# Kernel optimization log

Measured on AMD Instinct MI355X. Metric: run time of the kernel, lower is better.

Reference implementation:

```python
import jax, jax.numpy as jnp
import numpy as np

IN_F, OUT_F = 1024, 1024
GRID_SIZE, SPLINE_ORDER = 5, 3
GRID_RANGE = (-1.0, 1.0)
NUM_BASIS = GRID_SIZE + SPLINE_ORDER  # 8


def b_splines(x, grid, spline_order):
    # x: (B, in), grid: (in, G) with G = grid_size + 2*spline_order + 1
    x = x[..., None]            # (B, in, 1)
    g = grid[None, :, :]        # (1, in, G)
    B = ((x >= g[..., :-1]) & (x < g[..., 1:])).astype(x.dtype)  # (B, in, G-1)
    for k in range(1, spline_order + 1):
        left = (x - g[..., :-(k + 1)]) / (g[..., k:-1] - g[..., :-(k + 1)])
        right = (g[..., k + 1:] - x) / (g[..., k + 1:] - g[..., 1:-k])
        B = left * B[..., :-1] + right * B[..., 1:]
    return B  # (B, in, grid_size + spline_order)


def setup_inputs() -> dict:
    key = jax.random.key(0)
    k1, k2, k3, k4 = jax.random.split(key, 4)
    batch = 8192
    x = jax.random.normal(k1, (batch, IN_F), dtype=jnp.float32)
    h = (GRID_RANGE[1] - GRID_RANGE[0]) / GRID_SIZE
    knots = jnp.arange(-SPLINE_ORDER, GRID_SIZE + SPLINE_ORDER + 1, dtype=jnp.float32) * h + GRID_RANGE[0]
    grid = jnp.broadcast_to(knots, (IN_F, knots.shape[0]))  # (in, 12)
    base_weight = jax.random.normal(k2, (OUT_F, IN_F), dtype=jnp.float32) * (1.0 / np.sqrt(IN_F))
    spline_weight = jax.random.normal(k3, (OUT_F, IN_F, NUM_BASIS), dtype=jnp.float32) * 0.02
    spline_scaler = jax.random.normal(k4, (OUT_F, IN_F), dtype=jnp.float32) * (1.0 / np.sqrt(IN_F))
    return {"x": x, "grid": grid, "base_weight": base_weight,
            "spline_weight": spline_weight, "spline_scaler": spline_scaler}


def reference(x, grid, base_weight, spline_weight, spline_scaler):
    # base branch: SiLU then linear
    base_out = jax.nn.silu(x) @ base_weight.T  # (B, out)
    # normalize x to [-1, 1] by global min/max
    x_min, x_max = jnp.min(x), jnp.max(x)
    x_norm = (x - x_min) / (x_max - x_min + 1e-8) * 2.0 - 1.0
    basis = b_splines(x_norm, grid, SPLINE_ORDER)  # (B, in, K)
    w = spline_weight * spline_scaler[..., None]   # (out, in, K)
    spline_out = jnp.einsum('bik,oik->bo', basis, w)
    return base_out + spline_out
```

## Files before the change

kernel.cpp:

```cpp
#include <hip/hip_runtime.h>
#include <hip/hip_bf16.h>

#define IN_F   1024
#define OUT_F  1024
#define NBASIS 8
#define KDIM   (IN_F + IN_F * NBASIS)
#define BK 64
#define KT      (KDIM / BK)

#define BM3 128
#define BN3 256
#define A_ELEMS (BM3 * BK)
#define B_ELEMS (BN3 * BK)
#define SLOT    (A_ELEMS + B_ELEMS)
#define A_OFF   0
#define B_OFF   A_ELEMS

#define BM 128
#define BN 128

typedef __attribute__((ext_vector_type(8)))  short          bf16x8;
typedef __attribute__((ext_vector_type(8)))  unsigned short u16x8;
typedef __attribute__((ext_vector_type(4)))  float          f32x4;
typedef __attribute__((ext_vector_type(16))) float          f32x16;

typedef const __attribute__((address_space(1))) void gas_t;
typedef __attribute__((address_space(3))) void las_t;
#define GLD16(g, l) __builtin_amdgcn_global_load_lds((gas_t*)(g), (las_t*)(l), 16, 0, 0)

__device__ __forceinline__ unsigned short bfr(float f) {
    unsigned u = __float_as_uint(f);
    unsigned r = (u + 0x7FFFu + ((u >> 16) & 1u)) >> 16;
    return (unsigned short)r;
}
__device__ __forceinline__ float silu_f(float v) { return v / (1.0f + __expf(-v)); }

__device__ __forceinline__ unsigned fkey(float f) {
    unsigned u = __float_as_uint(f);
    return u ^ ((u >> 31) ? 0xFFFFFFFFu : 0x80000000u);
}
__device__ __forceinline__ float fkey_dec(unsigned u) {
    unsigned b = (u >> 31) ? (u ^ 0x80000000u) : ~u;
    return __uint_as_float(b);
}

__device__ __forceinline__ void spline8(float xv, float xmin, float scale, u16x8* o8p) {
    float xn = (xv - xmin) * scale - 1.0f;
    float u  = (xn + 2.2f) * 2.5f;
    int   iv = (int)floorf(u);
    iv = iv < 3 ? 3 : (iv > 7 ? 7 : iv);
    float tt = u - (float)iv;
    float s1 = 1.0f - tt;
    float t2 = tt * tt, t3 = t2 * tt;
    float n0 = s1 * s1 * s1 * (1.0f / 6.0f);
    float n1 = (3.0f * t3 - 6.0f * t2 + 4.0f) * (1.0f / 6.0f);
    float n2 = (-3.0f * t3 + 3.0f * t2 + 3.0f * tt + 1.0f) * (1.0f / 6.0f);
    float n3 = t3 * (1.0f / 6.0f);
    int j0 = iv - 3;
    u16x8 o8;
    #pragma unroll
    for (int s = 0; s < 8; ++s) {
        int d = s - j0;
        float val = (d == 0) ? n0 : (d == 1) ? n1 : (d == 2) ? n2 : (d == 3) ? n3 : 0.0f;
        o8[s] = bfr(val);
    }
    *o8p = o8;
}

__global__ void k_minmax(const float* __restrict__ x, unsigned* __restrict__ mm, int n4) {
    int tid    = blockIdx.x * blockDim.x + threadIdx.x;
    int stride = gridDim.x * blockDim.x;
    const float4* x4 = (const float4*)x;
    float mx  = -3.402823466e+38f;
    float mxn = -3.402823466e+38f;
    for (int i = tid; i < n4; i += stride) {
        float4 v = x4[i];
        mx  = fmaxf(mx,  fmaxf(fmaxf(v.x, v.y), fmaxf(v.z, v.w)));
        mxn = fmaxf(mxn, -fminf(fminf(v.x, v.y), fminf(v.z, v.w)));
    }
    #pragma unroll
    for (int off = 32; off; off >>= 1) {
        mx  = fmaxf(mx,  __shfl_down(mx,  off));
        mxn = fmaxf(mxn, __shfl_down(mxn, off));
    }
    __shared__ float smx[4], smn[4];
    int lane = threadIdx.x & 63, wid = threadIdx.x >> 6;
    if (lane == 0) { smx[wid] = mx; smn[wid] = mxn; }
    __syncthreads();
    if (threadIdx.x == 0) {
        #pragma unroll
        for (int w = 1; w < 4; ++w) { mx = fmaxf(mx, smx[w]); mxn = fmaxf(mxn, smn[w]); }
        atomicMax(&mm[0], fkey(mx));
        atomicMax(&mm[1], fkey(mxn));
    }
}

__global__ void k_prep_all(const float* __restrict__ x, const unsigned* __restrict__ mm,
                           const float* __restrict__ bw, const float* __restrict__ sw,
                           const float* __restrict__ sc,
                           unsigned short* __restrict__ Ac, unsigned short* __restrict__ Wc,
                           int nba) {
    int bid = blockIdx.x;
    if (bid < nba) {
        int t = bid * 256 + threadIdx.x;
        int row = t >> 10, i = t & 1023;
        const float xmax  = fkey_dec(mm[0]);
        const float xmin  = -fkey_dec(mm[1]);
        const float scale = 2.0f / (xmax - xmin + 1e-8f);
        float xv = x[t];
        size_t rb = (size_t)row * KDIM;
        Ac[rb + i] = bfr(silu_f(xv));
        u16x8 o8;
        spline8(xv, xmin, scale, &o8);
        *(u16x8*)(Ac + rb + IN_F + (size_t)i * 8) = o8;
    } else {
        int t = (bid - nba) * 256 + threadIdx.x;
        int o = t >> 10, i = t & 1023;
        Wc[(size_t)o * KDIM + i] = bfr(bw[t]);
        float s = sc[t];
        const float4* swv = (const float4*)(sw + (size_t)t * 8);
        float4 a = swv[0], b = swv[1];
        u16x8 o8;
        o8[0] = bfr(a.x * s); o8[1] = bfr(a.y * s); o8[2] = bfr(a.z * s); o8[3] = bfr(a.w * s);
        o8[4] = bfr(b.x * s); o8[5] = bfr(b.y * s); o8[6] = bfr(b.z * s); o8[7] = bfr(b.w * s);
        *(u16x8*)(Wc + (size_t)o * KDIM + IN_F + i * 8) = o8;
    }
}

#define MFMA32(a, b, c) __builtin_amdgcn_mfma_f32_32x32x16_bf16((a), (b), (c), 0, 0, 0)
#define MFMA16(a, b, c) __builtin_amdgcn_mfma_f32_16x16x32_bf16((a), (b), (c), 0, 0, 0)

__global__ __launch_bounds__(512, 2)
void k_gemm4(const unsigned short* __restrict__ Ac, const unsigned short* __restrict__ Wc,
             float* __restrict__ out) {
    __shared__ unsigned short sm[3 * SLOT];

    const int t    = threadIdx.x;
    const int lane = t & 63, w = t >> 6;
    const int bid  = blockIdx.x;
    const int xcd = bid & 7, s = bid >> 3;
    const int bM  = xcd * 8 + (s & 7);
    const int bN  = s >> 3;

    const int wave_r = w >> 2;
    const int wcq    = w & 3;
    const int l31 = lane & 31;
    const int hl  = lane >> 5;

    const unsigned short* pa0; const unsigned short* pa1;
    const unsigned short* pb0; const unsigned short* pb1;
    const unsigned short* pb2; const unsigned short* pb3;
    {
        int L, r, c;
        L = (0 * 8 + w) * 64 + lane; r = L >> 3; c = L & 7;
        pa0 = Ac + (size_t)(bM * BM3 + r) * KDIM + (c ^ (r & 7)) * 8;
        L = (1 * 8 + w) * 64 + lane; r = L >> 3; c = L & 7;
        pa1 = Ac + (size_t)(bM * BM3 + r) * KDIM + (c ^ (r & 7)) * 8;
        L = (0 * 8 + w) * 64 + lane; r = L >> 3; c = L & 7;
        pb0 = Wc + (size_t)(bN * BN3 + r) * KDIM + (c ^ (r & 7)) * 8;
        L = (1 * 8 + w) * 64 + lane; r = L >> 3; c = L & 7;
        pb1 = Wc + (size_t)(bN * BN3 + r) * KDIM + (c ^ (r & 7)) * 8;
        L = (2 * 8 + w) * 64 + lane; r = L >> 3; c = L & 7;
        pb2 = Wc + (size_t)(bN * BN3 + r) * KDIM + (c ^ (r & 7)) * 8;
        L = (3 * 8 + w) * 64 + lane; r = L >> 3; c = L & 7;
        pb3 = Wc + (size_t)(bN * BN3 + r) * KDIM + (c ^ (r & 7)) * 8;
    }

    int rA[2], rB[2];
    #pragma unroll
    for (int mi = 0; mi < 2; ++mi) rA[mi] = wave_r * 64 + mi * 32 + l31;
    #pragma unroll
    for (int ni = 0; ni < 2; ++ni) rB[ni] = wcq * 64 + ni * 32 + l31;

    f32x16 acc[2][2] = {};

    GLD16(pa0, &sm[0 * SLOT + A_OFF + (0 * 8 + w) * 512]);
    GLD16(pa1, &sm[0 * SLOT + A_OFF + (1 * 8 + w) * 512]);
    GLD16(pb0, &sm[0 * SLOT + B_OFF + (0 * 8 + w) * 512]);
    GLD16(pb1, &sm[0 * SLOT + B_OFF + (1 * 8 + w) * 512]);
    GLD16(pb2, &sm[0 * SLOT + B_OFF + (2 * 8 + w) * 512]);
    GLD16(pb3, &sm[0 * SLOT + B_OFF + (3 * 8 + w) * 512]);
    pa0 += BK; pa1 += BK; pb0 += BK; pb1 += BK; pb2 += BK; pb3 += BK;
    GLD16(pa0, &sm[1 * SLOT + A_OFF + (0 * 8 + w) * 512]);
    GLD16(pa1, &sm[1 * SLOT + A_OFF + (1 * 8 + w) * 512]);
    GLD16(pb0, &sm[1 * SLOT + B_OFF + (0 * 8 + w) * 512]);
    GLD16(pb1, &sm[1 * SLOT + B_OFF + (1 * 8 + w) * 512]);
    GLD16(pb2, &sm[1 * SLOT + B_OFF + (2 * 8 + w) * 512]);
    GLD16(pb3, &sm[1 * SLOT + B_OFF + (3 * 8 + w) * 512]);
    pa0 += BK; pa1 += BK; pb0 += BK; pb1 += BK; pb2 += BK; pb3 += BK;

    int o0 = 0, o1 = SLOT, o2 = 2 * SLOT;
    int sk = 2;

    asm volatile("s_waitcnt vmcnt(6)" ::: "memory");
    asm volatile("s_barrier" ::: "memory");

    for (int kt = 0; kt < KT; ++kt) {
        {
            bf16x8 a0[2], a1[2], b0[2], b1[2];
            #pragma unroll
            for (int mi = 0; mi < 2; ++mi) {
                int sa = rA[mi] & 7;
                a0[mi] = *(const bf16x8*)&sm[o0 + A_OFF + rA[mi] * BK + (((0 + hl) ^ sa) << 3)];
                a1[mi] = *(const bf16x8*)&sm[o0 + A_OFF + rA[mi] * BK + (((2 + hl) ^ sa) << 3)];
            }
            #pragma unroll
            for (int ni = 0; ni < 2; ++ni) {
                int sb = rB[ni] & 7;
                b0[ni] = *(const bf16x8*)&sm[o0 + B_OFF + rB[ni] * BK + (((0 + hl) ^ sb) << 3)];
                b1[ni] = *(const bf16x8*)&sm[o0 + B_OFF + rB[ni] * BK + (((2 + hl) ^ sb) << 3)];
            }
            GLD16(pa0, &sm[o2 + A_OFF + (0 * 8 + w) * 512]);
            GLD16(pa1, &sm[o2 + A_OFF + (1 * 8 + w) * 512]);
            __builtin_amdgcn_s_barrier();
            __builtin_amdgcn_s_setprio(1);
            #pragma unroll
            for (int mi = 0; mi < 2; ++mi)
                #pragma unroll
                for (int ni = 0; ni < 2; ++ni) {
                    acc[mi][ni] = MFMA32(a0[mi], b0[ni], acc[mi][ni]);
                    acc[mi][ni] = MFMA32(a1[mi], b1[ni], acc[mi][ni]);
                }
            __builtin_amdgcn_s_setprio(0);
            __builtin_amdgcn_s_barrier();
        }
        {
            bf16x8 a0[2], a1[2], b0[2], b1[2];
            #pragma unroll
            for (int mi = 0; mi < 2; ++mi) {
                int sa = rA[mi] & 7;
                a0[mi] = *(const bf16x8*)&sm[o0 + A_OFF + rA[mi] * BK + (((4 + hl) ^ sa) << 3)];
                a1[mi] = *(const bf16x8*)&sm[o0 + A_OFF + rA[mi] * BK + (((6 + hl) ^ sa) << 3)];
            }
            #pragma unroll
            for (int ni = 0; ni < 2; ++ni) {
                int sb = rB[ni] & 7;
                b0[ni] = *(const bf16x8*)&sm[o0 + B_OFF + rB[ni] * BK + (((4 + hl) ^ sb) << 3)];
                b1[ni] = *(const bf16x8*)&sm[o0 + B_OFF + rB[ni] * BK + (((6 + hl) ^ sb) << 3)];
            }
            GLD16(pb0, &sm[o2 + B_OFF + (0 * 8 + w) * 512]);
            GLD16(pb1, &sm[o2 + B_OFF + (1 * 8 + w) * 512]);
            GLD16(pb2, &sm[o2 + B_OFF + (2 * 8 + w) * 512]);
            GLD16(pb3, &sm[o2 + B_OFF + (3 * 8 + w) * 512]);
            __builtin_amdgcn_s_barrier();
            __builtin_amdgcn_s_setprio(1);
            #pragma unroll
            for (int mi = 0; mi < 2; ++mi)
                #pragma unroll
                for (int ni = 0; ni < 2; ++ni) {
                    acc[mi][ni] = MFMA32(a0[mi], b0[ni], acc[mi][ni]);
                    acc[mi][ni] = MFMA32(a1[mi], b1[ni], acc[mi][ni]);
                }
            __builtin_amdgcn_s_setprio(0);
        }

        pa0 += BK; pa1 += BK; pb0 += BK; pb1 += BK; pb2 += BK; pb3 += BK;
        if (++sk == KT) {
            sk = 0;
            pa0 -= KDIM; pa1 -= KDIM; pb0 -= KDIM; pb1 -= KDIM; pb2 -= KDIM; pb3 -= KDIM;
        }

        asm volatile("s_waitcnt vmcnt(6)" ::: "memory");
        asm volatile("s_barrier" ::: "memory");
        int tmp = o0; o0 = o1; o1 = o2; o2 = tmp;
    }

    #pragma unroll
    for (int mi = 0; mi < 2; ++mi) {
        #pragma unroll
        for (int ni = 0; ni < 2; ++ni) {
            #pragma unroll
            for (int reg = 0; reg < 16; ++reg) {
                int row = bM * BM3 + wave_r * 64 + mi * 32 + (reg & 3) + 8 * (reg >> 2) + 4 * hl;
                int col = bN * BN3 + wcq * 64 + ni * 32 + l31;
                out[(size_t)row * OUT_F + col] = acc[mi][ni][reg];
            }
        }
    }
}

__global__ __launch_bounds__(256, 2)
void k_gemm2(const unsigned short* __restrict__ Ac, const unsigned short* __restrict__ Wc,
             float* __restrict__ out, int nmb) {
    __shared__ unsigned short As[BM * BK];
    __shared__ unsigned short Bs[BN * BK];

    const int t = threadIdx.x;
    const int lane = t & 63, w = t >> 6;
    int bid = blockIdx.x;
    int bM = bid >> 3, bN = bid & 7;

    const unsigned short* pa[4];
    const unsigned short* pb[4];
    #pragma unroll
    for (int q = 0; q < 4; ++q) {
        int idx = (q * 4 + w) * 64 + lane;
        int r = idx >> 3, c8 = idx & 7;
        pa[q] = Ac + (size_t)(bM * BM + r) * KDIM + c8 * 8;
        pb[q] = Wc + (size_t)(bN * BN + r) * KDIM + c8 * 8;
    }

    const int wr  = (w >> 1) * 64;
    const int wc2 = (w & 1) * 64;

    f32x4 acc[4][4] = {};

    for (int kt = 0; kt < KT; ++kt) {
        __syncthreads();
        #pragma unroll
        for (int q = 0; q < 4; ++q) {
            GLD16(pa[q], &As[(q * 4 + w) * 512]);
            GLD16(pb[q], &Bs[(q * 4 + w) * 512]);
            pa[q] += BK;
            pb[q] += BK;
        }
        __syncthreads();

        bf16x8 af[4][2];
        #pragma unroll
        for (int mi = 0; mi < 4; ++mi) {
            int row = wr + mi * 16 + (lane & 15);
            #pragma unroll
            for (int ks = 0; ks < 2; ++ks)
                af[mi][ks] = *(const bf16x8*)&As[row * BK + ks * 32 + (lane >> 4) * 8];
        }
        #pragma unroll
        for (int ni = 0; ni < 4; ++ni) {
            int col = wc2 + ni * 16 + (lane & 15);
            bf16x8 b0 = *(const bf16x8*)&Bs[col * BK + (lane >> 4) * 8];
            bf16x8 b1 = *(const bf16x8*)&Bs[col * BK + 32 + (lane >> 4) * 8];
            #pragma unroll
            for (int mi = 0; mi < 4; ++mi) {
                acc[mi][ni] = MFMA16(af[mi][0], b0, acc[mi][ni]);
                acc[mi][ni] = MFMA16(af[mi][1], b1, acc[mi][ni]);
            }
        }
    }

    #pragma unroll
    for (int mi = 0; mi < 4; ++mi) {
        #pragma unroll
        for (int ni = 0; ni < 4; ++ni) {
            #pragma unroll
            for (int reg = 0; reg < 4; ++reg) {
                int row = wr + mi * 16 + (lane >> 4) * 4 + reg;
                int col = wc2 + ni * 16 + (lane & 15);
                out[(size_t)(bM * BM + row) * OUT_F + bN * BN + col] = acc[mi][ni][reg];
            }
        }
    }
}

extern "C" void kernel_launch(void* const* d_in, const int* in_sizes, int n_in,
                              void* d_out, int out_size, void* d_ws, size_t ws_size,
                              hipStream_t stream) {
    const float* x  = (const float*)d_in[0];
    const float* bw = (const float*)d_in[2];
    const float* sw = (const float*)d_in[3];
    const float* sc = (const float*)d_in[4];
    float* out = (float*)d_out;

    const int batch = in_sizes[0] / IN_F;
    const int n4    = in_sizes[0] / 4;

    unsigned*       mm = (unsigned*)d_ws;
    unsigned short* Wc = (unsigned short*)((char*)d_ws + 512);
    const size_t    wc_bytes = (size_t)OUT_F * KDIM * 2;
    unsigned short* Ac = (unsigned short*)((char*)d_ws + 512 + wc_bytes);
    const size_t    ac_bytes = (size_t)batch * KDIM * 2;
    const size_t    need = 512 + wc_bytes + ac_bytes;

    hipMemsetAsync(d_ws, 0, 8, stream);
    k_minmax<<<1024, 256, 0, stream>>>(x, mm, n4);

    const int nba = (batch * IN_F) / 256;
    k_prep_all<<<nba + (OUT_F * IN_F) / 256, 256, 0, stream>>>(x, mm, bw, sw, sc, Ac, Wc, nba);

    if (ws_size >= need && batch == 8192) {
        k_gemm4<<<dim3((batch / BM3) * (OUT_F / BN3)), 512, 0, stream>>>(Ac, Wc, out);
    } else if (ws_size >= need && (batch % BM) == 0) {
        k_gemm2<<<dim3((batch / BM) * (OUT_F / BN)), 256, 0, stream>>>(Ac, Wc, out, batch / BM);
    }
}
```

Measured before the change: 319.9 us.

## Load A fragments directly to registers and switch to 16x16 MFMA tiles

Replaces the GEMM kernel with a variant that no longer stages the activation tile through LDS. Each wave instead loads its A fragments straight from global memory into double-buffered registers one k-step ahead. Only the weight tile still goes through a triple-buffered LDS ring via global_load_lds. The MFMA shape changes from 32x32x16 to 16x16x32, with a 4x4 accumulator grid per wave, and the second mid-iteration barrier is removed. The aim is to cut LDS traffic and synchronisation, at the cost of duplicated A reads across the four column waves, which leans on L1/L2, and higher register pressure.

```diff
diff --git a/kernel.cpp b/kernel.cpp
--- a/kernel.cpp
+++ b/kernel.cpp
@@ -10,11 +10,7 @@
 
 #define BM3 128
 #define BN3 256
-#define A_ELEMS (BM3 * BK)
 #define B_ELEMS (BN3 * BK)
-#define SLOT    (A_ELEMS + B_ELEMS)
-#define A_OFF   0
-#define B_OFF   A_ELEMS
 
 #define BM 128
 #define BN 128
@@ -22,7 +18,6 @@
 typedef __attribute__((ext_vector_type(8)))  short          bf16x8;
 typedef __attribute__((ext_vector_type(8)))  unsigned short u16x8;
 typedef __attribute__((ext_vector_type(4)))  float          f32x4;
-typedef __attribute__((ext_vector_type(16))) float          f32x16;
 
 typedef const __attribute__((address_space(1))) void gas_t;
 typedef __attribute__((address_space(3))) void las_t;
@@ -127,13 +122,49 @@
     }
 }
 
-#define MFMA32(a, b, c) __builtin_amdgcn_mfma_f32_32x32x16_bf16((a), (b), (c), 0, 0, 0)
 #define MFMA16(a, b, c) __builtin_amdgcn_mfma_f32_16x16x32_bf16((a), (b), (c), 0, 0, 0)
 
+#define GEMM_BODY(AFC, AFN, KTCUR)                                              \
+    {                                                                           \
+        _Pragma("unroll")                                                       \
+        for (int q = 0; q < 4; ++q) GLD16(pb[q], &Bs[o2 + (q * 8 + w) * 512]);  \
+        _Pragma("unroll")                                                       \
+        for (int q = 0; q < 4; ++q) pb[q] += BK;                                \
+        if (++sk == KT) { sk = 0;                                               \
+            _Pragma("unroll")                                                   \
+            for (int q = 0; q < 4; ++q) pb[q] -= KDIM; }                        \
+        int an = (KTCUR) + 1; if (an == KT) an = 0;                             \
+        const unsigned short* ap = aBase + (size_t)an * BK;                     \
+        _Pragma("unroll")                                                       \
+        for (int mi = 0; mi < 4; ++mi) {                                        \
+            AFN[mi][0] = *(const bf16x8*)(ap + mi * aMi);                       \
+            AFN[mi][1] = *(const bf16x8*)(ap + mi * aMi + 32);                  \
+        }                                                                       \
+        bf16x8 bf[4][2];                                                        \
+        _Pragma("unroll")                                                       \
+        for (int ni = 0; ni < 4; ++ni) {                                        \
+            int r = wcq * 64 + ni * 16 + l15;                                   \
+            bf[ni][0] = *(const bf16x8*)&Bs[o0 + r * BK + ach0 * 8];            \
+            bf[ni][1] = *(const bf16x8*)&Bs[o0 + r * BK + ach1 * 8];            \
+        }                                                                       \
+        __builtin_amdgcn_s_setprio(1);                                          \
+        _Pragma("unroll")                                                       \
+        for (int ni = 0; ni < 4; ++ni)                                          \
+            _Pragma("unroll")                                                   \
+            for (int mi = 0; mi < 4; ++mi) {                                    \
+                acc[mi][ni] = MFMA16(AFC[mi][0], bf[ni][0], acc[mi][ni]);       \
+                acc[mi][ni] = MFMA16(AFC[mi][1], bf[ni][1], acc[mi][ni]);       \
+            }                                                                   \
+        __builtin_amdgcn_s_setprio(0);                                          \
+        asm volatile("s_waitcnt vmcnt(12)" ::: "memory");                       \
+        asm volatile("s_barrier" ::: "memory");                                 \
+        int _tmp = o0; o0 = o1; o1 = o2; o2 = _tmp;                             \
+    }
+
 __global__ __launch_bounds__(512, 2)
-void k_gemm4(const unsigned short* __restrict__ Ac, const unsigned short* __restrict__ Wc,
+void k_gemm5(const unsigned short* __restrict__ Ac, const unsigned short* __restrict__ Wc,
              float* __restrict__ out) {
-    __shared__ unsigned short sm[3 * SLOT];
+    __shared__ unsigned short Bs[3 * B_ELEMS];
 
     const int t    = threadIdx.x;
     const int lane = t & 63, w = t >> 6;
@@ -144,135 +175,56 @@
 
     const int wave_r = w >> 2;
     const int wcq    = w & 3;
-    const int l31 = lane & 31;
-    const int hl  = lane >> 5;
-
-    const unsigned short* pa0; const unsigned short* pa1;
-    const unsigned short* pb0; const unsigned short* pb1;
-    const unsigned short* pb2; const unsigned short* pb3;
-    {
-        int L, r, c;
-        L = (0 * 8 + w) * 64 + lane; r = L >> 3; c = L & 7;
-        pa0 = Ac + (size_t)(bM * BM3 + r) * KDIM + (c ^ (r & 7)) * 8;
-        L = (1 * 8 + w) * 64 + lane; r = L >> 3; c = L & 7;
-        pa1 = Ac + (size_t)(bM * BM3 + r) * KDIM + (c ^ (r & 7)) * 8;
-        L = (0 * 8 + w) * 64 + lane; r = L >> 3; c = L & 7;
-        pb0 = Wc + (size_t)(bN * BN3 + r) * KDIM + (c ^ (r & 7)) * 8;
-        L = (1 * 8 + w) * 64 + lane; r = L >> 3; c = L & 7;
-        pb1 = Wc + (size_t)(bN * BN3 + r) * KDIM + (c ^ (r & 7)) * 8;
-        L = (2 * 8 + w) * 64 + lane; r = L >> 3; c = L & 7;
-        pb2 = Wc + (size_t)(bN * BN3 + r) * KDIM + (c ^ (r & 7)) * 8;
-        L = (3 * 8 + w) * 64 + lane; r = L >> 3; c = L & 7;
-        pb3 = Wc + (size_t)(bN * BN3 + r) * KDIM + (c ^ (r & 7)) * 8;
-    }
-
-    int rA[2], rB[2];
-    #pragma unroll
-    for (int mi = 0; mi < 2; ++mi) rA[mi] = wave_r * 64 + mi * 32 + l31;
-    #pragma unroll
-    for (int ni = 0; ni < 2; ++ni) rB[ni] = wcq * 64 + ni * 32 + l31;
-
-    f32x16 acc[2][2] = {};
-
-    GLD16(pa0, &sm[0 * SLOT + A_OFF + (0 * 8 + w) * 512]);
-    GLD16(pa1, &sm[0 * SLOT + A_OFF + (1 * 8 + w) * 512]);
-    GLD16(pb0, &sm[0 * SLOT + B_OFF + (0 * 8 + w) * 512]);
-    GLD16(pb1, &sm[0 * SLOT + B_OFF + (1 * 8 + w) * 512]);
-    GLD16(pb2, &sm[0 * SLOT + B_OFF + (2 * 8 + w) * 512]);
-    GLD16(pb3, &sm[0 * SLOT + B_OFF + (3 * 8 + w) * 512]);
-    pa0 += BK; pa1 += BK; pb0 += BK; pb1 += BK; pb2 += BK; pb3 += BK;
-    GLD16(pa0, &sm[1 * SLOT + A_OFF + (0 * 8 + w) * 512]);
-    GLD16(pa1, &sm[1 * SLOT + A_OFF + (1 * 8 + w) * 512]);
-    GLD16(pb0, &sm[1 * SLOT + B_OFF + (0 * 8 + w) * 512]);
-    GLD16(pb1, &sm[1 * SLOT + B_OFF + (1 * 8 + w) * 512]);
-    GLD16(pb2, &sm[1 * SLOT + B_OFF + (2 * 8 + w) * 512]);
-    GLD16(pb3, &sm[1 * SLOT + B_OFF + (3 * 8 + w) * 512]);
-    pa0 += BK; pa1 += BK; pb0 += BK; pb1 += BK; pb2 += BK; pb3 += BK;
-
-    int o0 = 0, o1 = SLOT, o2 = 2 * SLOT;
+    const int l15  = lane & 15;
+    const int ach0 = (lane >> 4) ^ (lane & 7);
+    const int ach1 = ach0 ^ 4;
+
+    const unsigned short* pb[4];
+    #pragma unroll
+    for (int q = 0; q < 4; ++q) {
+        int L = (q * 8 + w) * 64 + lane;
+        int r = L >> 3, c = L & 7;
+        pb[q] = Wc + (size_t)(bN * BN3 + r) * KDIM + (c ^ (r & 7)) * 8;
+    }
+
+    const unsigned short* aBase =
+        Ac + (size_t)(bM * BM3 + wave_r * 64 + l15) * KDIM + (lane >> 4) * 8;
+    const size_t aMi = (size_t)16 * KDIM;
+
+    f32x4 acc[4][4] = {};
+    bf16x8 afA[4][2], afB[4][2];
+
+    #pragma unroll
+    for (int q = 0; q < 4; ++q) GLD16(pb[q], &Bs[0 * B_ELEMS + (q * 8 + w) * 512]);
+    #pragma unroll
+    for (int q = 0; q < 4; ++q) GLD16(pb[q] + BK, &Bs[1 * B_ELEMS + (q * 8 + w) * 512]);
+    #pragma unroll
+    for (int mi = 0; mi < 4; ++mi) {
+        afA[mi][0] = *(const bf16x8*)(aBase + mi * aMi);
+        afA[mi][1] = *(const bf16x8*)(aBase + mi * aMi + 32);
+    }
+    #pragma unroll
+    for (int q = 0; q < 4; ++q) pb[q] += 2 * BK;
+
+    int o0 = 0, o1 = B_ELEMS, o2 = 2 * B_ELEMS;
     int sk = 2;
 
-    asm volatile("s_waitcnt vmcnt(6)" ::: "memory");
+    asm volatile("s_waitcnt vmcnt(12)" ::: "memory");
     asm volatile("s_barrier" ::: "memory");
 
-    for (int kt = 0; kt < KT; ++kt) {
-        {
-            bf16x8 a0[2], a1[2], b0[2], b1[2];
+    for (int kt = 0; kt < KT; kt += 2) {
+        GEMM_BODY(afA, afB, kt)
+        GEMM_BODY(afB, afA, kt + 1)
+    }
+
+    #pragma unroll
+    for (int mi = 0; mi < 4; ++mi) {
+        #pragma unroll
+        for (int ni = 0; ni < 4; ++ni) {
             #pragma unroll
-            for (int mi = 0; mi < 2; ++mi) {
-                int sa = rA[mi] & 7;
-                a0[mi] = *(const bf16x8*)&sm[o0 + A_OFF + rA[mi] * BK + (((0 + hl) ^ sa) << 3)];
-                a1[mi] = *(const bf16x8*)&sm[o0 + A_OFF + rA[mi] * BK + (((2 + hl) ^ sa) << 3)];
-            }
-            #pragma unroll
-            for (int ni = 0; ni < 2; ++ni) {
-                int sb = rB[ni] & 7;
-                b0[ni] = *(const bf16x8*)&sm[o0 + B_OFF + rB[ni] * BK + (((0 + hl) ^ sb) << 3)];
-                b1[ni] = *(const bf16x8*)&sm[o0 + B_OFF + rB[ni] * BK + (((2 + hl) ^ sb) << 3)];
-            }
-            GLD16(pa0, &sm[o2 + A_OFF + (0 * 8 + w) * 512]);
-            GLD16(pa1, &sm[o2 + A_OFF + (1 * 8 + w) * 512]);
-            __builtin_amdgcn_s_barrier();
-            __builtin_amdgcn_s_setprio(1);
-            #pragma unroll
-            for (int mi = 0; mi < 2; ++mi)
-                #pragma unroll
-                for (int ni = 0; ni < 2; ++ni) {
-                    acc[mi][ni] = MFMA32(a0[mi], b0[ni], acc[mi][ni]);
-                    acc[mi][ni] = MFMA32(a1[mi], b1[ni], acc[mi][ni]);
-                }
-            __builtin_amdgcn_s_setprio(0);
-            __builtin_amdgcn_s_barrier();
-        }
-        {
-            bf16x8 a0[2], a1[2], b0[2], b1[2];
-            #pragma unroll
-            for (int mi = 0; mi < 2; ++mi) {
-                int sa = rA[mi] & 7;
-                a0[mi] = *(const bf16x8*)&sm[o0 + A_OFF + rA[mi] * BK + (((4 + hl) ^ sa) << 3)];
-                a1[mi] = *(const bf16x8*)&sm[o0 + A_OFF + rA[mi] * BK + (((6 + hl) ^ sa) << 3)];
-            }
-            #pragma unroll
-            for (int ni = 0; ni < 2; ++ni) {
-                int sb = rB[ni] & 7;
-                b0[ni] = *(const bf16x8*)&sm[o0 + B_OFF + rB[ni] * BK + (((4 + hl) ^ sb) << 3)];
-                b1[ni] = *(const bf16x8*)&sm[o0 + B_OFF + rB[ni] * BK + (((6 + hl) ^ sb) << 3)];
-            }
-            GLD16(pb0, &sm[o2 + B_OFF + (0 * 8 + w) * 512]);
-            GLD16(pb1, &sm[o2 + B_OFF + (1 * 8 + w) * 512]);
-            GLD16(pb2, &sm[o2 + B_OFF + (2 * 8 + w) * 512]);
-            GLD16(pb3, &sm[o2 + B_OFF + (3 * 8 + w) * 512]);
-            __builtin_amdgcn_s_barrier();
-            __builtin_amdgcn_s_setprio(1);
-            #pragma unroll
-            for (int mi = 0; mi < 2; ++mi)
-                #pragma unroll
-                for (int ni = 0; ni < 2; ++ni) {
-                    acc[mi][ni] = MFMA32(a0[mi], b0[ni], acc[mi][ni]);
-                    acc[mi][ni] = MFMA32(a1[mi], b1[ni], acc[mi][ni]);
-                }
-            __builtin_amdgcn_s_setprio(0);
-        }
-
-        pa0 += BK; pa1 += BK; pb0 += BK; pb1 += BK; pb2 += BK; pb3 += BK;
-        if (++sk == KT) {
-            sk = 0;
-            pa0 -= KDIM; pa1 -= KDIM; pb0 -= KDIM; pb1 -= KDIM; pb2 -= KDIM; pb3 -= KDIM;
-        }
-
-        asm volatile("s_waitcnt vmcnt(6)" ::: "memory");
-        asm volatile("s_barrier" ::: "memory");
-        int tmp = o0; o0 = o1; o1 = o2; o2 = tmp;
-    }
-
-    #pragma unroll
-    for (int mi = 0; mi < 2; ++mi) {
-        #pragma unroll
-        for (int ni = 0; ni < 2; ++ni) {
-            #pragma unroll
-            for (int reg = 0; reg < 16; ++reg) {
-                int row = bM * BM3 + wave_r * 64 + mi * 32 + (reg & 3) + 8 * (reg >> 2) + 4 * hl;
-                int col = bN * BN3 + wcq * 64 + ni * 32 + l31;
+            for (int reg = 0; reg < 4; ++reg) {
+                int row = bM * BM3 + wave_r * 64 + mi * 16 + (lane >> 4) * 4 + reg;
+                int col = bN * BN3 + wcq * 64 + ni * 16 + l15;
                 out[(size_t)row * OUT_F + col] = acc[mi][ni][reg];
             }
         }
@@ -377,7 +329,7 @@
     k_prep_all<<<nba + (OUT_F * IN_F) / 256, 256, 0, stream>>>(x, mm, bw, sw, sc, Ac, Wc, nba);
 
     if (ws_size >= need && batch == 8192) {
-        k_gemm4<<<dim3((batch / BM3) * (OUT_F / BN3)), 512, 0, stream>>>(Ac, Wc, out);
+        k_gemm5<<<dim3((batch / BM3) * (OUT_F / BN3)), 512, 0, stream>>>(Ac, Wc, out);
     } else if (ws_size >= need && (batch % BM) == 0) {
         k_gemm2<<<dim3((batch / BM) * (OUT_F / BN)), 256, 0, stream>>>(Ac, Wc, out, batch / BM);
     }
```

Result: slower. 497.5 us (+55.5%).

## Switch main GEMM to 16x16x32 MFMA tiles with four-phase K loop

Applied to the files above, without the earlier changes.

Replaces the 32x32x16 bf16 MFMA inner loop with 16x16x32 MFMAs. Each wave computes its 64x64 tile as a 4x4 grid of 16x16 accumulators, and each K tile is split into four barrier-separated phases that interleave LDS fragment reads with the global-to-LDS prefetches. A fragments are reused across two phases. The aim is better instruction interleaving and LDS read patterns, at the cost of more barriers, more MFMA issues and a different accumulator and output layout.

```diff
diff --git a/kernel.cpp b/kernel.cpp
--- a/kernel.cpp
+++ b/kernel.cpp
@@ -22,7 +22,6 @@
 typedef __attribute__((ext_vector_type(8)))  short          bf16x8;
 typedef __attribute__((ext_vector_type(8)))  unsigned short u16x8;
 typedef __attribute__((ext_vector_type(4)))  float          f32x4;
-typedef __attribute__((ext_vector_type(16))) float          f32x16;
 
 typedef const __attribute__((address_space(1))) void gas_t;
 typedef __attribute__((address_space(3))) void las_t;
@@ -127,11 +126,10 @@
     }
 }
 
-#define MFMA32(a, b, c) __builtin_amdgcn_mfma_f32_32x32x16_bf16((a), (b), (c), 0, 0, 0)
 #define MFMA16(a, b, c) __builtin_amdgcn_mfma_f32_16x16x32_bf16((a), (b), (c), 0, 0, 0)
 
 __global__ __launch_bounds__(512, 2)
-void k_gemm4(const unsigned short* __restrict__ Ac, const unsigned short* __restrict__ Wc,
+void k_gemm6(const unsigned short* __restrict__ Ac, const unsigned short* __restrict__ Wc,
              float* __restrict__ out) {
     __shared__ unsigned short sm[3 * SLOT];
 
@@ -144,8 +142,9 @@
 
     const int wave_r = w >> 2;
     const int wcq    = w & 3;
-    const int l31 = lane & 31;
-    const int hl  = lane >> 5;
+    const int l15  = lane & 15;
+    const int ach0 = (lane >> 4) ^ (lane & 7);
+    const int ach1 = ach0 ^ 4;
 
     const unsigned short* pa0; const unsigned short* pa1;
     const unsigned short* pb0; const unsigned short* pb1;
@@ -166,13 +165,7 @@
         pb3 = Wc + (size_t)(bN * BN3 + r) * KDIM + (c ^ (r & 7)) * 8;
     }
 
-    int rA[2], rB[2];
-    #pragma unroll
-    for (int mi = 0; mi < 2; ++mi) rA[mi] = wave_r * 64 + mi * 32 + l31;
-    #pragma unroll
-    for (int ni = 0; ni < 2; ++ni) rB[ni] = wcq * 64 + ni * 32 + l31;
-
-    f32x16 acc[2][2] = {};
+    f32x4 acc[4][4] = {};
 
     GLD16(pa0, &sm[0 * SLOT + A_OFF + (0 * 8 + w) * 512]);
     GLD16(pa1, &sm[0 * SLOT + A_OFF + (1 * 8 + w) * 512]);
@@ -196,61 +189,88 @@
     asm volatile("s_barrier" ::: "memory");
 
     for (int kt = 0; kt < KT; ++kt) {
+        bf16x8 af0[4], af1[4];
         {
-            bf16x8 a0[2], a1[2], b0[2], b1[2];
-            #pragma unroll
-            for (int mi = 0; mi < 2; ++mi) {
-                int sa = rA[mi] & 7;
-                a0[mi] = *(const bf16x8*)&sm[o0 + A_OFF + rA[mi] * BK + (((0 + hl) ^ sa) << 3)];
-                a1[mi] = *(const bf16x8*)&sm[o0 + A_OFF + rA[mi] * BK + (((2 + hl) ^ sa) << 3)];
-            }
+            #pragma unroll
+            for (int mi = 0; mi < 4; ++mi) {
+                int r = wave_r * 64 + mi * 16 + l15;
+                af0[mi] = *(const bf16x8*)&sm[o0 + A_OFF + r * BK + ach0 * 8];
+            }
+            bf16x8 bf[2];
             #pragma unroll
             for (int ni = 0; ni < 2; ++ni) {
-                int sb = rB[ni] & 7;
-                b0[ni] = *(const bf16x8*)&sm[o0 + B_OFF + rB[ni] * BK + (((0 + hl) ^ sb) << 3)];
-                b1[ni] = *(const bf16x8*)&sm[o0 + B_OFF + rB[ni] * BK + (((2 + hl) ^ sb) << 3)];
+                int r = wcq * 64 + ni * 16 + l15;
+                bf[ni] = *(const bf16x8*)&sm[o0 + B_OFF + r * BK + ach0 * 8];
             }
             GLD16(pa0, &sm[o2 + A_OFF + (0 * 8 + w) * 512]);
             GLD16(pa1, &sm[o2 + A_OFF + (1 * 8 + w) * 512]);
             __builtin_amdgcn_s_barrier();
             __builtin_amdgcn_s_setprio(1);
             #pragma unroll
-            for (int mi = 0; mi < 2; ++mi)
+            for (int ni = 0; ni < 2; ++ni)
                 #pragma unroll
-                for (int ni = 0; ni < 2; ++ni) {
-                    acc[mi][ni] = MFMA32(a0[mi], b0[ni], acc[mi][ni]);
-                    acc[mi][ni] = MFMA32(a1[mi], b1[ni], acc[mi][ni]);
-                }
+                for (int mi = 0; mi < 4; ++mi)
+                    acc[mi][ni] = MFMA16(af0[mi], bf[ni], acc[mi][ni]);
             __builtin_amdgcn_s_setprio(0);
             __builtin_amdgcn_s_barrier();
         }
         {
-            bf16x8 a0[2], a1[2], b0[2], b1[2];
-            #pragma unroll
-            for (int mi = 0; mi < 2; ++mi) {
-                int sa = rA[mi] & 7;
-                a0[mi] = *(const bf16x8*)&sm[o0 + A_OFF + rA[mi] * BK + (((4 + hl) ^ sa) << 3)];
-                a1[mi] = *(const bf16x8*)&sm[o0 + A_OFF + rA[mi] * BK + (((6 + hl) ^ sa) << 3)];
-            }
+            bf16x8 bf[2];
             #pragma unroll
             for (int ni = 0; ni < 2; ++ni) {
-                int sb = rB[ni] & 7;
-                b0[ni] = *(const bf16x8*)&sm[o0 + B_OFF + rB[ni] * BK + (((4 + hl) ^ sb) << 3)];
-                b1[ni] = *(const bf16x8*)&sm[o0 + B_OFF + rB[ni] * BK + (((6 + hl) ^ sb) << 3)];
+                int r = wcq * 64 + (ni + 2) * 16 + l15;
+                bf[ni] = *(const bf16x8*)&sm[o0 + B_OFF + r * BK + ach0 * 8];
             }
             GLD16(pb0, &sm[o2 + B_OFF + (0 * 8 + w) * 512]);
             GLD16(pb1, &sm[o2 + B_OFF + (1 * 8 + w) * 512]);
+            __builtin_amdgcn_s_barrier();
+            __builtin_amdgcn_s_setprio(1);
+            #pragma unroll
+            for (int ni = 0; ni < 2; ++ni)
+                #pragma unroll
+                for (int mi = 0; mi < 4; ++mi)
+                    acc[mi][ni + 2] = MFMA16(af0[mi], bf[ni], acc[mi][ni + 2]);
+            __builtin_amdgcn_s_setprio(0);
+            __builtin_amdgcn_s_barrier();
+        }
+        {
+            #pragma unroll
+            for (int mi = 0; mi < 4; ++mi) {
+                int r = wave_r * 64 + mi * 16 + l15;
+                af1[mi] = *(const bf16x8*)&sm[o0 + A_OFF + r * BK + ach1 * 8];
+            }
+            bf16x8 bf[2];
+            #pragma unroll
+            for (int ni = 0; ni < 2; ++ni) {
+                int r = wcq * 64 + ni * 16 + l15;
+                bf[ni] = *(const bf16x8*)&sm[o0 + B_OFF + r * BK + ach1 * 8];
+            }
             GLD16(pb2, &sm[o2 + B_OFF + (2 * 8 + w) * 512]);
             GLD16(pb3, &sm[o2 + B_OFF + (3 * 8 + w) * 512]);
             __builtin_amdgcn_s_barrier();
             __builtin_amdgcn_s_setprio(1);
             #pragma unroll
-            for (int mi = 0; mi < 2; ++mi)
+            for (int ni = 0; ni < 2; ++ni)
                 #pragma unroll
-                for (int ni = 0; ni < 2; ++ni) {
-                    acc[mi][ni] = MFMA32(a0[mi], b0[ni], acc[mi][ni]);
-                    acc[mi][ni] = MFMA32(a1[mi], b1[ni], acc[mi][ni]);
-                }
+                for (int mi = 0; mi < 4; ++mi)
+                    acc[mi][ni] = MFMA16(af1[mi], bf[ni], acc[mi][ni]);
+            __builtin_amdgcn_s_setprio(0);
+            __builtin_amdgcn_s_barrier();
+        }
+        {
+            bf16x8 bf[2];
+            #pragma unroll
+            for (int ni = 0; ni < 2; ++ni) {
+                int r = wcq * 64 + (ni + 2) * 16 + l15;
+                bf[ni] = *(const bf16x8*)&sm[o0 + B_OFF + r * BK + ach1 * 8];
+            }
+            __builtin_amdgcn_s_barrier();
+            __builtin_amdgcn_s_setprio(1);
+            #pragma unroll
+            for (int ni = 0; ni < 2; ++ni)
+                #pragma unroll
+                for (int mi = 0; mi < 4; ++mi)
+                    acc[mi][ni + 2] = MFMA16(af1[mi], bf[ni], acc[mi][ni + 2]);
             __builtin_amdgcn_s_setprio(0);
         }
 
@@ -266,13 +286,13 @@
     }
 
     #pragma unroll
-    for (int mi = 0; mi < 2; ++mi) {
-        #pragma unroll
-        for (int ni = 0; ni < 2; ++ni) {
-            #pragma unroll
-            for (int reg = 0; reg < 16; ++reg) {
-                int row = bM * BM3 + wave_r * 64 + mi * 32 + (reg & 3) + 8 * (reg >> 2) + 4 * hl;
-                int col = bN * BN3 + wcq * 64 + ni * 32 + l31;
+    for (int mi = 0; mi < 4; ++mi) {
+        #pragma unroll
+        for (int ni = 0; ni < 4; ++ni) {
+            #pragma unroll
+            for (int reg = 0; reg < 4; ++reg) {
+                int row = bM * BM3 + wave_r * 64 + mi * 16 + (lane >> 4) * 4 + reg;
+                int col = bN * BN3 + wcq * 64 + ni * 16 + l15;
                 out[(size_t)row * OUT_F + col] = acc[mi][ni][reg];
             }
         }
@@ -377,7 +397,7 @@
     k_prep_all<<<nba + (OUT_F * IN_F) / 256, 256, 0, stream>>>(x, mm, bw, sw, sc, Ac, Wc, nba);
 
     if (ws_size >= need && batch == 8192) {
-        k_gemm4<<<dim3((batch / BM3) * (OUT_F / BN3)), 512, 0, stream>>>(Ac, Wc, out);
+        k_gemm6<<<dim3((batch / BM3) * (OUT_F / BN3)), 512, 0, stream>>>(Ac, Wc, out);
     } else if (ws_size >= need && (batch % BM) == 0) {
         k_gemm2<<<dim3((batch / BM) * (OUT_F / BN)), 256, 0, stream>>>(Ac, Wc, out, batch / BM);
     }
```

After: 300.3 us. -6.1%, faster.
